# Performance work log

Hardware: AMD Instinct MI355X
Metric: run time of the kernel (lower is better)

## Reference

```python
import jax, jax.numpy as jnp
import numpy as np

N_NODES = 50000
N_EDGES = 800000
IN_DIM = 128
HID = 64
HEADS = 4
NEG_SLOPE = 0.2  # PyG GATConv default
EPS = 1e-16


def _glorot(key, shape):
    fan_in, fan_out = shape[0], shape[-1]
    lim = jnp.sqrt(6.0 / (fan_in + fan_out))
    return jax.random.uniform(key, shape, jnp.float32, -lim, lim)


def setup_inputs() -> dict:
    key = jax.random.key(0)
    ks = jax.random.split(key, 10)
    x = jax.random.normal(ks[0], (N_NODES, IN_DIM), jnp.float32)
    edge_index = jax.random.randint(ks[1], (2, N_EDGES), 0, N_NODES, jnp.int64)
    # Layer 1: in=128 -> 64 per head, 4 heads (concat -> 256)
    W1 = _glorot(ks[2], (IN_DIM, HEADS * HID))
    a_src1 = _glorot(ks[3], (HEADS, HID))
    a_dst1 = _glorot(ks[4], (HEADS, HID))
    b1 = jnp.zeros((HEADS * HID,), jnp.float32)
    # Layer 2: in=256 -> 1, 1 head
    W2 = _glorot(ks[5], (HEADS * HID, 1))
    a_src2 = _glorot(ks[6], (1, 1))
    a_dst2 = _glorot(ks[7], (1, 1))
    b2 = jnp.zeros((1,), jnp.float32)
    return {"x": x, "edge_index": edge_index, "W1": W1, "a_src1": a_src1,
            "a_dst1": a_dst1, "b1": b1, "W2": W2, "a_src2": a_src2,
            "a_dst2": a_dst2, "b2": b2}


def gat_conv(x, src, dst, W, a_src, a_dst, bias, heads, out_dim, num_nodes, concat):
    # Linear projection per head: [N, heads, out_dim]
    h = (x @ W).reshape(num_nodes, heads, out_dim)
    # Node-level attention logits: [N, heads]
    alpha_s = jnp.einsum('nhd,hd->nh', h, a_src)
    alpha_d = jnp.einsum('nhd,hd->nh', h, a_dst)
    # Per-edge score with LeakyReLU
    e = jax.nn.leaky_relu(alpha_s[src] + alpha_d[dst], NEG_SLOPE)  # [E, heads]
    # Segment softmax over incoming edges of each destination node
    e_max = jax.lax.stop_gradient(jax.ops.segment_max(e, dst, num_segments=num_nodes))
    e_exp = jnp.exp(e - e_max[dst])
    denom = jax.ops.segment_sum(e_exp, dst, num_segments=num_nodes)
    alpha = e_exp / (denom[dst] + EPS)  # [E, heads]
    # Weighted scatter-aggregate of source features
    msg = h[src] * alpha[:, :, None]  # [E, heads, out_dim]
    out = jax.ops.segment_sum(msg, dst, num_segments=num_nodes)
    if concat:
        out = out.reshape(num_nodes, heads * out_dim)
    else:
        out = out.mean(axis=1)
    return out + bias


def reference(x, edge_index, W1, a_src1, a_dst1, b1, W2, a_src2, a_dst2, b2):
    n = x.shape[0]
    loops = jnp.arange(n, dtype=edge_index.dtype)
    src = jnp.concatenate([edge_index[0], loops])  # PyG add_self_loops=True
    dst = jnp.concatenate([edge_index[1], loops])
    h = gat_conv(x, src, dst, W1, a_src1, a_dst1, b1, HEADS, HID, n, concat=True)
    h = jax.nn.relu(h)
    out = gat_conv(h, src, dst, W2, a_src2, a_dst2, b2, 1, 1, n, concat=True)
    return jax.nn.sigmoid(out)
```

## Files before the change

kernel.cpp:

```cpp
#include <hip/hip_runtime.h>
#include <hip/hip_bf16.h>

#define N_NODES 50000
#define N_EDGES 800000
#define ET      (N_EDGES + N_NODES)
#define IN_DIM  128
#define HID     64
#define HEADS   4
#define C1      (HEADS * HID)
#define NEG_SLOPE 0.2f

#define NBH     256
#define NBUCKET 196
#define SCAN_N  (NBUCKET * NBH)

typedef unsigned short ushort_t;
typedef __attribute__((ext_vector_type(8))) short bf16x8;
typedef __attribute__((ext_vector_type(4))) float f32x4;

__device__ __forceinline__ float asf(unsigned int u) {
    union { unsigned int i; float f; } c; c.i = u; return c.f;
}
__device__ __forceinline__ float bf2f(ushort_t u) {
    return asf(((unsigned int)u) << 16);
}
__device__ __forceinline__ ushort_t f2bf(float f) {
    union { float f; unsigned int i; } c; c.f = f;
    unsigned int r = c.i + 0x7fffu + ((c.i >> 16) & 1u);
    return (ushort_t)(r >> 16);
}
__device__ __forceinline__ float lrelu(float x) { return x > 0.f ? x : NEG_SLOPE * x; }

__device__ __forceinline__ float wave_sum(float v) {
    #pragma unroll
    for (int off = 32; off > 0; off >>= 1) v += __shfl_xor(v, off, 64);
    return v;
}
__device__ __forceinline__ int wave_sum_i(int v) {
    #pragma unroll
    for (int off = 32; off > 0; off >>= 1) v += __shfl_xor(v, off, 64);
    return v;
}

__device__ __forceinline__ int load_idx(const int* ei, int elem, int is64) {
    return is64 ? ei[2 * elem] : ei[elem];
}

__device__ __forceinline__ int detect64(const int* __restrict__ ei) {
    int lane = threadIdx.x & 63;
    unsigned long long nz = __ballot(lane < 32 && ei[2 * lane + 1] != 0);
    return nz == 0ull;
}

__global__ __launch_bounds__(256) void k_hist(const int* __restrict__ ei,
                                              int* __restrict__ HT) {
    __shared__ int lcnt[NBUCKET];
    int f = detect64(ei);
    if (threadIdx.x < NBUCKET) lcnt[threadIdx.x] = 0;
    __syncthreads();
    for (int e = blockIdx.x * 256 + threadIdx.x; e < ET; e += NBH * 256) {
        int d = (e < N_EDGES) ? load_idx(ei, N_EDGES + e, f) : e - N_EDGES;
        atomicAdd(&lcnt[d >> 8], 1);
    }
    __syncthreads();
    if (threadIdx.x < NBUCKET)
        HT[threadIdx.x * NBH + blockIdx.x] = lcnt[threadIdx.x];
}

__global__ __launch_bounds__(256) void k_blksum(const int* __restrict__ v,
                                                int* __restrict__ bsum) {
    int i = blockIdx.x * 256 + threadIdx.x;
    int s = wave_sum_i(v[i]);
    __shared__ int ws[4];
    int lane = threadIdx.x & 63, wid = threadIdx.x >> 6;
    if (lane == 0) ws[wid] = s;
    __syncthreads();
    if (threadIdx.x == 0) bsum[blockIdx.x] = ws[0] + ws[1] + ws[2] + ws[3];
}

__global__ __launch_bounds__(256) void k_bscan(const int* __restrict__ bsum,
                                               int* __restrict__ boff) {
    int tid = threadIdx.x, lane = tid & 63, wid = tid >> 6;
    int v = (tid < NBUCKET) ? bsum[tid] : 0;
    int x = v;
    #pragma unroll
    for (int off = 1; off < 64; off <<= 1) {
        int t = __shfl_up(x, off, 64);
        if (lane >= off) x += t;
    }
    __shared__ int ws[4];
    if (lane == 63) ws[wid] = x;
    __syncthreads();
    int add = 0;
    for (int w = 0; w < 4; ++w) if (w < wid) add += ws[w];
    x += add;
    if (tid < NBUCKET) boff[tid] = x - v;
}

__global__ __launch_bounds__(256) void k_apply(const int* __restrict__ v,
                                               const int* __restrict__ boff,
                                               int* __restrict__ out) {
    int i = blockIdx.x * 256 + threadIdx.x;
    int lane = threadIdx.x & 63, wid = threadIdx.x >> 6;
    int val = v[i];
    int x = val;
    #pragma unroll
    for (int off = 1; off < 64; off <<= 1) {
        int t = __shfl_up(x, off, 64);
        if (lane >= off) x += t;
    }
    __shared__ int ws[4];
    if (lane == 63) ws[wid] = x;
    __syncthreads();
    int add = boff[blockIdx.x];
    for (int w = 0; w < 4; ++w) if (w < wid) add += ws[w];
    out[i] = add + x - val;
}

__global__ __launch_bounds__(256) void k_bucket_scatter(const int* __restrict__ ei,
                                                        const int* __restrict__ HToff,
                                                        uint2* __restrict__ bucketed) {
    __shared__ int lbase[NBUCKET];
    int f = detect64(ei);
    if (threadIdx.x < NBUCKET)
        lbase[threadIdx.x] = HToff[threadIdx.x * NBH + blockIdx.x];
    __syncthreads();
    for (int e = blockIdx.x * 256 + threadIdx.x; e < ET; e += NBH * 256) {
        int s, d;
        if (e < N_EDGES) { s = load_idx(ei, e, f); d = load_idx(ei, N_EDGES + e, f); }
        else             { s = d = e - N_EDGES; }
        int pos = atomicAdd(&lbase[d >> 8], 1);
        bucketed[pos] = make_uint2((unsigned)s, (unsigned)d);
    }
}

__global__ __launch_bounds__(256) void k_fine(const uint2* __restrict__ bucketed,
                                              const int* __restrict__ HToff,
                                              int* __restrict__ row_start,
                                              int* __restrict__ edge_src) {
    __shared__ int fcnt[256];
    __shared__ int fcur[256];
    __shared__ int ws[4];
    int b = blockIdx.x, tid = threadIdx.x;
    int lane = tid & 63, wid = tid >> 6;
    int estart = HToff[b * NBH];
    int eend   = (b + 1 < NBUCKET) ? HToff[(b + 1) * NBH] : ET;
    fcnt[tid] = 0;
    __syncthreads();
    for (int i = estart + tid; i < eend; i += 256)
        atomicAdd(&fcnt[bucketed[i].y & 255], 1);
    __syncthreads();
    int v = fcnt[tid];
    int x = v;
    #pragma unroll
    for (int off = 1; off < 64; off <<= 1) {
        int t = __shfl_up(x, off, 64);
        if (lane >= off) x += t;
    }
    if (lane == 63) ws[wid] = x;
    __syncthreads();
    int add = 0;
    for (int w = 0; w < 4; ++w) if (w < wid) add += ws[w];
    int excl = add + x - v;
    int node = b * 256 + tid;
    if (node <= N_NODES) row_start[node] = estart + excl;
    fcur[tid] = estart + excl;
    __syncthreads();
    for (int i = estart + tid; i < eend; i += 256) {
        uint2 u = bucketed[i];
        int pos = atomicAdd(&fcur[u.y & 255], 1);
        edge_src[pos] = (int)u.x;
    }
}

__global__ void k_w1swz(const float* __restrict__ W1, ushort_t* __restrict__ w1s) {
    int o = blockIdx.x * 256 + threadIdx.x;
    int j = o & 7, l = (o >> 3) & 63, c = (o >> 9) & 3, t = o >> 11;
    int k = c * 32 + ((l >> 4) << 3) + j;
    int n = (t << 4) + (l & 15);
    w1s[o] = f2bf(W1[k * C1 + n]);
}

__global__ __launch_bounds__(256) void k_gemm1(const float* __restrict__ x,
                                               const ushort_t* __restrict__ w1s,
                                               const float* __restrict__ a_src1,
                                               const float* __restrict__ a_dst1,
                                               ushort_t* __restrict__ h1,
                                               float* __restrict__ as1,
                                               float* __restrict__ ad1) {
    int lane = threadIdx.x & 63;
    int wave = (blockIdx.x * 256 + threadIdx.x) >> 6;
    int row0 = wave * 16;
    if (row0 >= N_NODES) return;
    int quad = lane >> 4, mrow = lane & 15;

    f32x4 acc[16];
    #pragma unroll
    for (int t = 0; t < 16; ++t) acc[t] = (f32x4){0.f, 0.f, 0.f, 0.f};

    const float* xrow = x + (size_t)(row0 + mrow) * IN_DIM + quad * 8;
    #pragma unroll
    for (int c = 0; c < 4; ++c) {
        float4 xa = *(const float4*)(xrow + c * 32);
        float4 xb = *(const float4*)(xrow + c * 32 + 4);
        bf16x8 a;
        a[0] = (short)f2bf(xa.x); a[1] = (short)f2bf(xa.y);
        a[2] = (short)f2bf(xa.z); a[3] = (short)f2bf(xa.w);
        a[4] = (short)f2bf(xb.x); a[5] = (short)f2bf(xb.y);
        a[6] = (short)f2bf(xb.z); a[7] = (short)f2bf(xb.w);
        #pragma unroll
        for (int t = 0; t < 16; ++t) {
            bf16x8 b = *(const bf16x8*)(w1s + (((t * 4 + c) * 64 + lane) << 3));
            acc[t] = __builtin_amdgcn_mfma_f32_16x16x32_bf16(a, b, acc[t], 0, 0, 0);
        }
    }

    #pragma unroll
    for (int t = 0; t < 16; ++t) {
        int col = t * 16 + mrow;
        #pragma unroll
        for (int r = 0; r < 4; ++r) {
            h1[(size_t)(row0 + quad * 4 + r) * C1 + col] = f2bf(acc[t][r]);
        }
    }

    float asv[16], adv[16];
    #pragma unroll
    for (int t = 0; t < 16; ++t) {
        asv[t] = a_src1[t * 16 + mrow];
        adv[t] = a_dst1[t * 16 + mrow];
    }
    #pragma unroll
    for (int r = 0; r < 4; ++r) {
        float ps[4] = {0.f, 0.f, 0.f, 0.f};
        float pd[4] = {0.f, 0.f, 0.f, 0.f};
        #pragma unroll
        for (int t = 0; t < 16; ++t) {
            ps[t >> 2] += acc[t][r] * asv[t];
            pd[t >> 2] += acc[t][r] * adv[t];
        }
        #pragma unroll
        for (int h = 0; h < 4; ++h) {
            #pragma unroll
            for (int off = 1; off < 16; off <<= 1) {
                ps[h] += __shfl_xor(ps[h], off, 64);
                pd[h] += __shfl_xor(pd[h], off, 64);
            }
        }
        if (mrow == 0) {
            int rr = row0 + quad * 4 + r;
            #pragma unroll
            for (int h = 0; h < 4; ++h) {
                as1[rr * 4 + h] = ps[h];
                ad1[rr * 4 + h] = pd[h];
            }
        }
    }
}

__global__ __launch_bounds__(256) void k_agg1(const ushort_t* __restrict__ h1,
                                              const float* __restrict__ as1,
                                              const float* __restrict__ ad1,
                                              const int* __restrict__ row_start,
                                              const int* __restrict__ edge_src,
                                              const float* __restrict__ b1,
                                              const float* __restrict__ W2,
                                              const float* __restrict__ a_src2,
                                              const float* __restrict__ a_dst2,
                                              float2* __restrict__ pk,
                                              float* __restrict__ ad2) {
    __shared__ float wbuf[4][64][4];
    int lane = threadIdx.x & 63;
    int wid  = threadIdx.x >> 6;
    int node = blockIdx.x * 4 + wid;
    int rs = row_start[node], re = row_start[node + 1];
    float4 ad = *(const float4*)&ad1[node * 4];
    const int head = lane >> 4;

    float4 acc = make_float4(0.f, 0.f, 0.f, 0.f);
    float4 den = make_float4(0.f, 0.f, 0.f, 0.f);

    for (int base = rs; base < re; base += 64) {
        int i = base + lane;
        int s_l = 0;
        float4 w = make_float4(0.f, 0.f, 0.f, 0.f);
        if (i < re) {
            s_l = edge_src[i];
            float4 av = *(const float4*)&as1[s_l * 4];
            w.x = __expf(lrelu(av.x + ad.x));
            w.y = __expf(lrelu(av.y + ad.y));
            w.z = __expf(lrelu(av.z + ad.z));
            w.w = __expf(lrelu(av.w + ad.w));
        }
        den.x += w.x; den.y += w.y; den.z += w.z; den.w += w.w;
        *(float4*)&wbuf[wid][lane][0] = w;
        int m = re - base; if (m > 64) m = 64;
        int j = 0;
        for (; j + 4 <= m; j += 4) {
            int s0 = __builtin_amdgcn_readlane(s_l, j + 0);
            int s1 = __builtin_amdgcn_readlane(s_l, j + 1);
            int s2 = __builtin_amdgcn_readlane(s_l, j + 2);
            int s3 = __builtin_amdgcn_readlane(s_l, j + 3);
            uint2 p0 = *(const uint2*)(h1 + (size_t)s0 * C1 + lane * 4);
            uint2 p1 = *(const uint2*)(h1 + (size_t)s1 * C1 + lane * 4);
            uint2 p2 = *(const uint2*)(h1 + (size_t)s2 * C1 + lane * 4);
            uint2 p3 = *(const uint2*)(h1 + (size_t)s3 * C1 + lane * 4);
            float g0 = wbuf[wid][j + 0][head];
            float g1 = wbuf[wid][j + 1][head];
            float g2 = wbuf[wid][j + 2][head];
            float g3 = wbuf[wid][j + 3][head];
            acc.x += g0 * asf(p0.x << 16);
            acc.y += g0 * asf(p0.x & 0xffff0000u);
            acc.z += g0 * asf(p0.y << 16);
            acc.w += g0 * asf(p0.y & 0xffff0000u);
            acc.x += g1 * asf(p1.x << 16);
            acc.y += g1 * asf(p1.x & 0xffff0000u);
            acc.z += g1 * asf(p1.y << 16);
            acc.w += g1 * asf(p1.y & 0xffff0000u);
            acc.x += g2 * asf(p2.x << 16);
            acc.y += g2 * asf(p2.x & 0xffff0000u);
            acc.z += g2 * asf(p2.y << 16);
            acc.w += g2 * asf(p2.y & 0xffff0000u);
            acc.x += g3 * asf(p3.x << 16);
            acc.y += g3 * asf(p3.x & 0xffff0000u);
            acc.z += g3 * asf(p3.y << 16);
            acc.w += g3 * asf(p3.y & 0xffff0000u);
        }
        for (; j < m; ++j) {
            int s0 = __builtin_amdgcn_readlane(s_l, j);
            uint2 p0 = *(const uint2*)(h1 + (size_t)s0 * C1 + lane * 4);
            float g0 = wbuf[wid][j][head];
            acc.x += g0 * asf(p0.x << 16);
            acc.y += g0 * asf(p0.x & 0xffff0000u);
            acc.z += g0 * asf(p0.y << 16);
            acc.w += g0 * asf(p0.y & 0xffff0000u);
        }
    }

    float d0 = wave_sum(den.x), d1 = wave_sum(den.y);
    float d2 = wave_sum(den.z), d3 = wave_sum(den.w);
    float dh = head == 0 ? d0 : head == 1 ? d1 : head == 2 ? d2 : d3;
    float inv = 1.f / (dh + 1e-16f);
    float4 bv = *(const float4*)&b1[lane * 4];
    float o0 = fmaxf(acc.x * inv + bv.x, 0.f);
    float o1 = fmaxf(acc.y * inv + bv.y, 0.f);
    float o2 = fmaxf(acc.z * inv + bv.z, 0.f);
    float o3 = fmaxf(acc.w * inv + bv.w, 0.f);
    float4 wv = *(const float4*)&W2[lane * 4];
    float sum = o0 * wv.x + o1 * wv.y + o2 * wv.z + o3 * wv.w;
    sum = wave_sum(sum);
    if (lane == 0) {
        float2 p; p.x = sum * a_src2[0]; p.y = sum;
        pk[node]  = p;
        ad2[node] = sum * a_dst2[0];
    }
}

__global__ __launch_bounds__(256) void k_agg2(const float2* __restrict__ pk,
                                              const float* __restrict__ ad2,
                                              const int* __restrict__ row_start,
                                              const int* __restrict__ edge_src,
                                              const float* __restrict__ b2,
                                              float* __restrict__ outp) {
    int lane = threadIdx.x & 63;
    int node = blockIdx.x * 4 + (threadIdx.x >> 6);
    int rs = row_start[node], re = row_start[node + 1];
    float adv = ad2[node];
    float se = 0.f, wsm = 0.f;
    for (int i = rs + lane; i < re; i += 64) {
        int s = edge_src[i];
        float2 p = pk[s];
        float w = __expf(lrelu(p.x + adv));
        se += w; wsm += w * p.y;
    }
    se = wave_sum(se); wsm = wave_sum(wsm);
    if (lane == 0) {
        float v = wsm / (se + 1e-16f) + b2[0];
        outp[node] = 1.f / (1.f + __expf(-v));
    }
}

extern "C" void kernel_launch(void* const* d_in, const int* in_sizes, int n_in,
                              void* d_out, int out_size, void* d_ws, size_t ws_size,
                              hipStream_t stream) {
    (void)in_sizes; (void)n_in; (void)out_size; (void)ws_size;
    const float* x      = (const float*)d_in[0];
    const int*   ei     = (const int*)  d_in[1];
    const float* W1     = (const float*)d_in[2];
    const float* a_src1 = (const float*)d_in[3];
    const float* a_dst1 = (const float*)d_in[4];
    const float* b1     = (const float*)d_in[5];
    const float* W2     = (const float*)d_in[6];
    const float* a_src2 = (const float*)d_in[7];
    const float* a_dst2 = (const float*)d_in[8];
    const float* b2     = (const float*)d_in[9];
    float* out = (float*)d_out;

    char* w = (char*)d_ws;
    size_t off = 0;
    auto alloc = [&](size_t bytes) {
        void* p = w + off; off += (bytes + 255) & ~(size_t)255; return p;
    };
    ushort_t* h1       = (ushort_t*)alloc((size_t)N_NODES * C1 * 2);
    ushort_t* w1s      = (ushort_t*)alloc((size_t)IN_DIM * C1 * 2);
    float*    as1      = (float*)   alloc((size_t)N_NODES * 4 * 4);
    float*    ad1      = (float*)   alloc((size_t)N_NODES * 4 * 4);
    float2*   pk       = (float2*)  alloc((size_t)N_NODES * 8);
    float*    ad2      = (float*)   alloc((size_t)N_NODES * 4);
    int*      row_start= (int*)     alloc((size_t)(N_NODES + 1) * 4);
    int*      edge_src = (int*)     alloc((size_t)ET * 4);
    uint2*    bucketed = (uint2*)   alloc((size_t)ET * 8);
    int*      HT       = (int*)     alloc((size_t)SCAN_N * 4);
    int*      HToff    = (int*)     alloc((size_t)SCAN_N * 4);
    int*      bsum     = (int*)     alloc((size_t)NBUCKET * 4);
    int*      boff     = (int*)     alloc((size_t)NBUCKET * 4);

    k_hist<<<NBH, 256, 0, stream>>>(ei, HT);
    k_blksum<<<NBUCKET, 256, 0, stream>>>(HT, bsum);
    k_bscan<<<1, 256, 0, stream>>>(bsum, boff);
    k_apply<<<NBUCKET, 256, 0, stream>>>(HT, boff, HToff);
    k_bucket_scatter<<<NBH, 256, 0, stream>>>(ei, HToff, bucketed);
    k_fine<<<NBUCKET, 256, 0, stream>>>(bucketed, HToff, row_start, edge_src);

    k_w1swz<<<(IN_DIM * C1) / 256, 256, 0, stream>>>(W1, w1s);
    int nwave = (N_NODES + 15) / 16;
    k_gemm1<<<(nwave + 3) / 4, 256, 0, stream>>>(x, w1s, a_src1, a_dst1, h1, as1, ad1);
    k_agg1<<<N_NODES / 4, 256, 0, stream>>>(h1, as1, ad1, row_start, edge_src,
                                            b1, W2, a_src2, a_dst2, pk, ad2);
    k_agg2<<<N_NODES / 4, 256, 0, stream>>>(pk, ad2, row_start, edge_src, b2, out);
}
```

Before: 212.0 us.

## Precompute edge softmax weights in the CSR fine pass and fold the W1 swizzle into histogram

Edge attention weights (exp of leaky-relu logits) and per-node inverse softmax denominators are now computed inside k_fine, run after gemm1 with 512 threads. Each edge's four weights go to a float4 array; denominators are summed with LDS float atomics. k_agg1 then reads precomputed weights instead of gathering as1 and computing exp, and its inner gather loop is unrolled from 4 to 8. The W1 bf16 swizzle moves into k_hist to drop a launch. In exchange, roughly 27 MB of extra per-edge weight traffic is written and read back. k_fine, now running only 196 blocks, takes on the random as1 gathers and the atomics.

```diff
diff --git a/kernel.cpp b/kernel.cpp
--- a/kernel.cpp
+++ b/kernel.cpp
@@ -53,10 +53,19 @@
 }
 
 __global__ __launch_bounds__(256) void k_hist(const int* __restrict__ ei,
-                                              int* __restrict__ HT) {
+                                              int* __restrict__ HT,
+                                              const float* __restrict__ W1,
+                                              ushort_t* __restrict__ w1s) {
     __shared__ int lcnt[NBUCKET];
     int f = detect64(ei);
     if (threadIdx.x < NBUCKET) lcnt[threadIdx.x] = 0;
+    if (threadIdx.x < 128) {
+        int o = blockIdx.x * 128 + threadIdx.x;
+        int j = o & 7, l = (o >> 3) & 63, c = (o >> 9) & 3, t = o >> 11;
+        int k = c * 32 + ((l >> 4) << 3) + j;
+        int n = (t << 4) + (l & 15);
+        w1s[o] = f2bf(W1[k * C1 + n]);
+    }
     __syncthreads();
     for (int e = blockIdx.x * 256 + threadIdx.x; e < ET; e += NBH * 256) {
         int d = (e < N_EDGES) ? load_idx(ei, N_EDGES + e, f) : e - N_EDGES;
@@ -134,51 +143,81 @@
     }
 }
 
-__global__ __launch_bounds__(256) void k_fine(const uint2* __restrict__ bucketed,
+__global__ __launch_bounds__(512) void k_fine(const uint2* __restrict__ bucketed,
                                               const int* __restrict__ HToff,
+                                              const float* __restrict__ as1,
+                                              const float* __restrict__ ad1,
                                               int* __restrict__ row_start,
-                                              int* __restrict__ edge_src) {
+                                              int* __restrict__ edge_src,
+                                              float4* __restrict__ w4,
+                                              float* __restrict__ invden) {
     __shared__ int fcnt[256];
     __shared__ int fcur[256];
+    __shared__ float den[256][4];
     __shared__ int ws[4];
     int b = blockIdx.x, tid = threadIdx.x;
-    int lane = tid & 63, wid = tid >> 6;
     int estart = HToff[b * NBH];
     int eend   = (b + 1 < NBUCKET) ? HToff[(b + 1) * NBH] : ET;
-    fcnt[tid] = 0;
-    __syncthreads();
-    for (int i = estart + tid; i < eend; i += 256)
+    if (tid < 256) {
+        fcnt[tid] = 0;
+        den[tid][0] = 0.f; den[tid][1] = 0.f; den[tid][2] = 0.f; den[tid][3] = 0.f;
+    }
+    __syncthreads();
+    for (int i = estart + tid; i < eend; i += 512)
         atomicAdd(&fcnt[bucketed[i].y & 255], 1);
     __syncthreads();
-    int v = fcnt[tid];
-    int x = v;
-    #pragma unroll
-    for (int off = 1; off < 64; off <<= 1) {
-        int t = __shfl_up(x, off, 64);
-        if (lane >= off) x += t;
-    }
-    if (lane == 63) ws[wid] = x;
-    __syncthreads();
-    int add = 0;
-    for (int w = 0; w < 4; ++w) if (w < wid) add += ws[w];
-    int excl = add + x - v;
-    int node = b * 256 + tid;
-    if (node <= N_NODES) row_start[node] = estart + excl;
-    fcur[tid] = estart + excl;
-    __syncthreads();
-    for (int i = estart + tid; i < eend; i += 256) {
+    if (tid < 256) {
+        int lane = tid & 63, wid = tid >> 6;
+        int v = fcnt[tid];
+        int x = v;
+        #pragma unroll
+        for (int off = 1; off < 64; off <<= 1) {
+            int t = __shfl_up(x, off, 64);
+            if (lane >= off) x += t;
+        }
+        if (lane == 63) ws[wid] = x;
+        __syncthreads();
+        int add = 0;
+        for (int w = 0; w < 4; ++w) if (w < wid) add += ws[w];
+        int excl = add + x - v;
+        int node = b * 256 + tid;
+        if (node <= N_NODES) row_start[node] = estart + excl;
+        fcur[tid] = estart + excl;
+    } else {
+        __syncthreads();
+    }
+    __syncthreads();
+    for (int i = estart + tid; i < eend; i += 512) {
         uint2 u = bucketed[i];
-        int pos = atomicAdd(&fcur[u.y & 255], 1);
-        edge_src[pos] = (int)u.x;
-    }
-}
-
-__global__ void k_w1swz(const float* __restrict__ W1, ushort_t* __restrict__ w1s) {
-    int o = blockIdx.x * 256 + threadIdx.x;
-    int j = o & 7, l = (o >> 3) & 63, c = (o >> 9) & 3, t = o >> 11;
-    int k = c * 32 + ((l >> 4) << 3) + j;
-    int n = (t << 4) + (l & 15);
-    w1s[o] = f2bf(W1[k * C1 + n]);
+        int loc = u.y & 255;
+        int pos = atomicAdd(&fcur[loc], 1);
+        int s = (int)u.x;
+        float4 av = *(const float4*)&as1[s * 4];
+        float4 dv = *(const float4*)&ad1[(size_t)u.y * 4];
+        float4 wv;
+        wv.x = __expf(lrelu(av.x + dv.x));
+        wv.y = __expf(lrelu(av.y + dv.y));
+        wv.z = __expf(lrelu(av.z + dv.z));
+        wv.w = __expf(lrelu(av.w + dv.w));
+        w4[pos] = wv;
+        edge_src[pos] = s;
+        atomicAdd(&den[loc][0], wv.x);
+        atomicAdd(&den[loc][1], wv.y);
+        atomicAdd(&den[loc][2], wv.z);
+        atomicAdd(&den[loc][3], wv.w);
+    }
+    __syncthreads();
+    if (tid < 256) {
+        int node = b * 256 + tid;
+        if (node < N_NODES) {
+            float4 iv;
+            iv.x = 1.f / (den[tid][0] + 1e-16f);
+            iv.y = 1.f / (den[tid][1] + 1e-16f);
+            iv.z = 1.f / (den[tid][2] + 1e-16f);
+            iv.w = 1.f / (den[tid][3] + 1e-16f);
+            *(float4*)&invden[(size_t)node * 4] = iv;
+        }
+    }
 }
 
 __global__ __launch_bounds__(256) void k_gemm1(const float* __restrict__ x,
@@ -259,10 +298,10 @@
 }
 
 __global__ __launch_bounds__(256) void k_agg1(const ushort_t* __restrict__ h1,
-                                              const float* __restrict__ as1,
-                                              const float* __restrict__ ad1,
                                               const int* __restrict__ row_start,
                                               const int* __restrict__ edge_src,
+                                              const float4* __restrict__ w4,
+                                              const float* __restrict__ invden,
                                               const float* __restrict__ b1,
                                               const float* __restrict__ W2,
                                               const float* __restrict__ a_src2,
@@ -274,57 +313,34 @@
     int wid  = threadIdx.x >> 6;
     int node = blockIdx.x * 4 + wid;
     int rs = row_start[node], re = row_start[node + 1];
-    float4 ad = *(const float4*)&ad1[node * 4];
     const int head = lane >> 4;
 
     float4 acc = make_float4(0.f, 0.f, 0.f, 0.f);
-    float4 den = make_float4(0.f, 0.f, 0.f, 0.f);
 
     for (int base = rs; base < re; base += 64) {
         int i = base + lane;
         int s_l = 0;
-        float4 w = make_float4(0.f, 0.f, 0.f, 0.f);
-        if (i < re) {
-            s_l = edge_src[i];
-            float4 av = *(const float4*)&as1[s_l * 4];
-            w.x = __expf(lrelu(av.x + ad.x));
-            w.y = __expf(lrelu(av.y + ad.y));
-            w.z = __expf(lrelu(av.z + ad.z));
-            w.w = __expf(lrelu(av.w + ad.w));
-        }
-        den.x += w.x; den.y += w.y; den.z += w.z; den.w += w.w;
-        *(float4*)&wbuf[wid][lane][0] = w;
+        float4 wv = make_float4(0.f, 0.f, 0.f, 0.f);
+        if (i < re) { s_l = edge_src[i]; wv = w4[i]; }
+        *(float4*)&wbuf[wid][lane][0] = wv;
         int m = re - base; if (m > 64) m = 64;
         int j = 0;
-        for (; j + 4 <= m; j += 4) {
-            int s0 = __builtin_amdgcn_readlane(s_l, j + 0);
-            int s1 = __builtin_amdgcn_readlane(s_l, j + 1);
-            int s2 = __builtin_amdgcn_readlane(s_l, j + 2);
-            int s3 = __builtin_amdgcn_readlane(s_l, j + 3);
-            uint2 p0 = *(const uint2*)(h1 + (size_t)s0 * C1 + lane * 4);
-            uint2 p1 = *(const uint2*)(h1 + (size_t)s1 * C1 + lane * 4);
-            uint2 p2 = *(const uint2*)(h1 + (size_t)s2 * C1 + lane * 4);
-            uint2 p3 = *(const uint2*)(h1 + (size_t)s3 * C1 + lane * 4);
-            float g0 = wbuf[wid][j + 0][head];
-            float g1 = wbuf[wid][j + 1][head];
-            float g2 = wbuf[wid][j + 2][head];
-            float g3 = wbuf[wid][j + 3][head];
-            acc.x += g0 * asf(p0.x << 16);
-            acc.y += g0 * asf(p0.x & 0xffff0000u);
-            acc.z += g0 * asf(p0.y << 16);
-            acc.w += g0 * asf(p0.y & 0xffff0000u);
-            acc.x += g1 * asf(p1.x << 16);
-            acc.y += g1 * asf(p1.x & 0xffff0000u);
-            acc.z += g1 * asf(p1.y << 16);
-            acc.w += g1 * asf(p1.y & 0xffff0000u);
-            acc.x += g2 * asf(p2.x << 16);
-            acc.y += g2 * asf(p2.x & 0xffff0000u);
-            acc.z += g2 * asf(p2.y << 16);
-            acc.w += g2 * asf(p2.y & 0xffff0000u);
-            acc.x += g3 * asf(p3.x << 16);
-            acc.y += g3 * asf(p3.x & 0xffff0000u);
-            acc.z += g3 * asf(p3.y << 16);
-            acc.w += g3 * asf(p3.y & 0xffff0000u);
+        for (; j + 8 <= m; j += 8) {
+            int ss[8]; uint2 pp[8]; float gg[8];
+            #pragma unroll
+            for (int q = 0; q < 8; ++q) ss[q] = __builtin_amdgcn_readlane(s_l, j + q);
+            #pragma unroll
+            for (int q = 0; q < 8; ++q) {
+                pp[q] = *(const uint2*)(h1 + (size_t)ss[q] * C1 + lane * 4);
+                gg[q] = wbuf[wid][j + q][head];
+            }
+            #pragma unroll
+            for (int q = 0; q < 8; ++q) {
+                acc.x += gg[q] * asf(pp[q].x << 16);
+                acc.y += gg[q] * asf(pp[q].x & 0xffff0000u);
+                acc.z += gg[q] * asf(pp[q].y << 16);
+                acc.w += gg[q] * asf(pp[q].y & 0xffff0000u);
+            }
         }
         for (; j < m; ++j) {
             int s0 = __builtin_amdgcn_readlane(s_l, j);
@@ -337,17 +353,14 @@
         }
     }
 
-    float d0 = wave_sum(den.x), d1 = wave_sum(den.y);
-    float d2 = wave_sum(den.z), d3 = wave_sum(den.w);
-    float dh = head == 0 ? d0 : head == 1 ? d1 : head == 2 ? d2 : d3;
-    float inv = 1.f / (dh + 1e-16f);
+    float inv = invden[(size_t)node * 4 + head];
     float4 bv = *(const float4*)&b1[lane * 4];
     float o0 = fmaxf(acc.x * inv + bv.x, 0.f);
     float o1 = fmaxf(acc.y * inv + bv.y, 0.f);
     float o2 = fmaxf(acc.z * inv + bv.z, 0.f);
     float o3 = fmaxf(acc.w * inv + bv.w, 0.f);
-    float4 wv = *(const float4*)&W2[lane * 4];
-    float sum = o0 * wv.x + o1 * wv.y + o2 * wv.z + o3 * wv.w;
+    float4 wv2 = *(const float4*)&W2[lane * 4];
+    float sum = o0 * wv2.x + o1 * wv2.y + o2 * wv2.z + o3 * wv2.w;
     sum = wave_sum(sum);
     if (lane == 0) {
         float2 p; p.x = sum * a_src2[0]; p.y = sum;
@@ -405,27 +418,29 @@
     ushort_t* w1s      = (ushort_t*)alloc((size_t)IN_DIM * C1 * 2);
     float*    as1      = (float*)   alloc((size_t)N_NODES * 4 * 4);
     float*    ad1      = (float*)   alloc((size_t)N_NODES * 4 * 4);
+    float*    invden   = (float*)   alloc((size_t)N_NODES * 4 * 4);
     float2*   pk       = (float2*)  alloc((size_t)N_NODES * 8);
     float*    ad2      = (float*)   alloc((size_t)N_NODES * 4);
     int*      row_start= (int*)     alloc((size_t)(N_NODES + 1) * 4);
     int*      edge_src = (int*)     alloc((size_t)ET * 4);
+    float4*   w4       = (float4*)  alloc((size_t)ET * 16);
     uint2*    bucketed = (uint2*)   alloc((size_t)ET * 8);
     int*      HT       = (int*)     alloc((size_t)SCAN_N * 4);
     int*      HToff    = (int*)     alloc((size_t)SCAN_N * 4);
     int*      bsum     = (int*)     alloc((size_t)NBUCKET * 4);
     int*      boff     = (int*)     alloc((size_t)NBUCKET * 4);
 
-    k_hist<<<NBH, 256, 0, stream>>>(ei, HT);
+    k_hist<<<NBH, 256, 0, stream>>>(ei, HT, W1, w1s);
     k_blksum<<<NBUCKET, 256, 0, stream>>>(HT, bsum);
     k_bscan<<<1, 256, 0, stream>>>(bsum, boff);
     k_apply<<<NBUCKET, 256, 0, stream>>>(HT, boff, HToff);
     k_bucket_scatter<<<NBH, 256, 0, stream>>>(ei, HToff, bucketed);
-    k_fine<<<NBUCKET, 256, 0, stream>>>(bucketed, HToff, row_start, edge_src);
-
-    k_w1swz<<<(IN_DIM * C1) / 256, 256, 0, stream>>>(W1, w1s);
+
     int nwave = (N_NODES + 15) / 16;
     k_gemm1<<<(nwave + 3) / 4, 256, 0, stream>>>(x, w1s, a_src1, a_dst1, h1, as1, ad1);
-    k_agg1<<<N_NODES / 4, 256, 0, stream>>>(h1, as1, ad1, row_start, edge_src,
+    k_fine<<<NBUCKET, 512, 0, stream>>>(bucketed, HToff, as1, ad1,
+                                        row_start, edge_src, w4, invden);
+    k_agg1<<<N_NODES / 4, 256, 0, stream>>>(h1, row_start, edge_src, w4, invden,
                                             b1, W2, a_src2, a_dst2, pk, ad2);
     k_agg2<<<N_NODES / 4, 256, 0, stream>>>(pk, ad2, row_start, edge_src, b2, out);
 }
```

New measurement: 224.2 us. +5.8%, slower.

## Split agg1 gather into half-waves with 16-byte loads; fold W1 swizzle into histogram

Applied to the files above, without the earlier changes.

The layer-1 aggregation now assigns each half-wave to a different edge. Each lane loads 8 bf16 features with a 16-byte load, so a wave gathers two source rows per step and keeps up to eight edges in flight per unrolled iteration. The two halves' partial sums are combined with a cross-half shuffle, and the final wave sum is halved to undo the duplication. Separately, the W1 bf16 swizzle is moved into the histogram kernel to remove one launch. The odd-edge tail reads padding lanes that carry zero weight, which costs extra loads but keeps the result correct.

```diff
diff --git a/kernel.cpp b/kernel.cpp
--- a/kernel.cpp
+++ b/kernel.cpp
@@ -53,10 +53,19 @@
 }
 
 __global__ __launch_bounds__(256) void k_hist(const int* __restrict__ ei,
-                                              int* __restrict__ HT) {
+                                              int* __restrict__ HT,
+                                              const float* __restrict__ W1,
+                                              ushort_t* __restrict__ w1s) {
     __shared__ int lcnt[NBUCKET];
     int f = detect64(ei);
     if (threadIdx.x < NBUCKET) lcnt[threadIdx.x] = 0;
+    if (threadIdx.x < 128) {
+        int o = blockIdx.x * 128 + threadIdx.x;
+        int j = o & 7, l = (o >> 3) & 63, c = (o >> 9) & 3, t = o >> 11;
+        int k = c * 32 + ((l >> 4) << 3) + j;
+        int n = (t << 4) + (l & 15);
+        w1s[o] = f2bf(W1[k * C1 + n]);
+    }
     __syncthreads();
     for (int e = blockIdx.x * 256 + threadIdx.x; e < ET; e += NBH * 256) {
         int d = (e < N_EDGES) ? load_idx(ei, N_EDGES + e, f) : e - N_EDGES;
@@ -171,14 +180,6 @@
         int pos = atomicAdd(&fcur[u.y & 255], 1);
         edge_src[pos] = (int)u.x;
     }
-}
-
-__global__ void k_w1swz(const float* __restrict__ W1, ushort_t* __restrict__ w1s) {
-    int o = blockIdx.x * 256 + threadIdx.x;
-    int j = o & 7, l = (o >> 3) & 63, c = (o >> 9) & 3, t = o >> 11;
-    int k = c * 32 + ((l >> 4) << 3) + j;
-    int n = (t << 4) + (l & 15);
-    w1s[o] = f2bf(W1[k * C1 + n]);
 }
 
 __global__ __launch_bounds__(256) void k_gemm1(const float* __restrict__ x,
@@ -275,9 +276,11 @@
     int node = blockIdx.x * 4 + wid;
     int rs = row_start[node], re = row_start[node + 1];
     float4 ad = *(const float4*)&ad1[node * 4];
-    const int head = lane >> 4;
-
-    float4 acc = make_float4(0.f, 0.f, 0.f, 0.f);
+    const int lane32 = lane & 31;
+    const int half   = lane >> 5;
+    const int head8  = lane32 >> 3;
+
+    float acc[8] = {0.f, 0.f, 0.f, 0.f, 0.f, 0.f, 0.f, 0.f};
     float4 den = make_float4(0.f, 0.f, 0.f, 0.f);
 
     for (int base = rs; base < re; base += 64) {
@@ -296,59 +299,71 @@
         *(float4*)&wbuf[wid][lane][0] = w;
         int m = re - base; if (m > 64) m = 64;
         int j = 0;
-        for (; j + 4 <= m; j += 4) {
-            int s0 = __builtin_amdgcn_readlane(s_l, j + 0);
+        for (; j + 8 <= m; j += 8) {
+            int sp[4]; uint4 pp[4]; float gg[4];
+            #pragma unroll
+            for (int q = 0; q < 4; ++q) {
+                int s0 = __builtin_amdgcn_readlane(s_l, j + 2 * q);
+                int s1 = __builtin_amdgcn_readlane(s_l, j + 2 * q + 1);
+                sp[q] = half ? s1 : s0;
+            }
+            #pragma unroll
+            for (int q = 0; q < 4; ++q) {
+                pp[q] = *(const uint4*)(h1 + (size_t)sp[q] * C1 + lane32 * 8);
+                gg[q] = wbuf[wid][j + 2 * q + half][head8];
+            }
+            #pragma unroll
+            for (int q = 0; q < 4; ++q) {
+                acc[0] += gg[q] * asf(pp[q].x << 16);
+                acc[1] += gg[q] * asf(pp[q].x & 0xffff0000u);
+                acc[2] += gg[q] * asf(pp[q].y << 16);
+                acc[3] += gg[q] * asf(pp[q].y & 0xffff0000u);
+                acc[4] += gg[q] * asf(pp[q].z << 16);
+                acc[5] += gg[q] * asf(pp[q].z & 0xffff0000u);
+                acc[6] += gg[q] * asf(pp[q].w << 16);
+                acc[7] += gg[q] * asf(pp[q].w & 0xffff0000u);
+            }
+        }
+        for (; j < m; j += 2) {
+            int s0 = __builtin_amdgcn_readlane(s_l, j);
             int s1 = __builtin_amdgcn_readlane(s_l, j + 1);
-            int s2 = __builtin_amdgcn_readlane(s_l, j + 2);
-            int s3 = __builtin_amdgcn_readlane(s_l, j + 3);
-            uint2 p0 = *(const uint2*)(h1 + (size_t)s0 * C1 + lane * 4);
-            uint2 p1 = *(const uint2*)(h1 + (size_t)s1 * C1 + lane * 4);
-            uint2 p2 = *(const uint2*)(h1 + (size_t)s2 * C1 + lane * 4);
-            uint2 p3 = *(const uint2*)(h1 + (size_t)s3 * C1 + lane * 4);
-            float g0 = wbuf[wid][j + 0][head];
-            float g1 = wbuf[wid][j + 1][head];
-            float g2 = wbuf[wid][j + 2][head];
-            float g3 = wbuf[wid][j + 3][head];
-            acc.x += g0 * asf(p0.x << 16);
-            acc.y += g0 * asf(p0.x & 0xffff0000u);
-            acc.z += g0 * asf(p0.y << 16);
-            acc.w += g0 * asf(p0.y & 0xffff0000u);
-            acc.x += g1 * asf(p1.x << 16);
-            acc.y += g1 * asf(p1.x & 0xffff0000u);
-            acc.z += g1 * asf(p1.y << 16);
-            acc.w += g1 * asf(p1.y & 0xffff0000u);
-            acc.x += g2 * asf(p2.x << 16);
-            acc.y += g2 * asf(p2.x & 0xffff0000u);
-            acc.z += g2 * asf(p2.y << 16);
-            acc.w += g2 * asf(p2.y & 0xffff0000u);
-            acc.x += g3 * asf(p3.x << 16);
-            acc.y += g3 * asf(p3.x & 0xffff0000u);
-            acc.z += g3 * asf(p3.y << 16);
-            acc.w += g3 * asf(p3.y & 0xffff0000u);
-        }
-        for (; j < m; ++j) {
-            int s0 = __builtin_amdgcn_readlane(s_l, j);
-            uint2 p0 = *(const uint2*)(h1 + (size_t)s0 * C1 + lane * 4);
-            float g0 = wbuf[wid][j][head];
-            acc.x += g0 * asf(p0.x << 16);
-            acc.y += g0 * asf(p0.x & 0xffff0000u);
-            acc.z += g0 * asf(p0.y << 16);
-            acc.w += g0 * asf(p0.y & 0xffff0000u);
-        }
-    }
+            int sp = half ? s1 : s0;
+            uint4 p0 = *(const uint4*)(h1 + (size_t)sp * C1 + lane32 * 8);
+            float g0 = wbuf[wid][j + half][head8];
+            acc[0] += g0 * asf(p0.x << 16);
+            acc[1] += g0 * asf(p0.x & 0xffff0000u);
+            acc[2] += g0 * asf(p0.y << 16);
+            acc[3] += g0 * asf(p0.y & 0xffff0000u);
+            acc[4] += g0 * asf(p0.z << 16);
+            acc[5] += g0 * asf(p0.z & 0xffff0000u);
+            acc[6] += g0 * asf(p0.w << 16);
+            acc[7] += g0 * asf(p0.w & 0xffff0000u);
+        }
+    }
+
+    #pragma unroll
+    for (int i2 = 0; i2 < 8; ++i2) acc[i2] += __shfl_xor(acc[i2], 32, 64);
 
     float d0 = wave_sum(den.x), d1 = wave_sum(den.y);
     float d2 = wave_sum(den.z), d3 = wave_sum(den.w);
-    float dh = head == 0 ? d0 : head == 1 ? d1 : head == 2 ? d2 : d3;
+    float dh = head8 == 0 ? d0 : head8 == 1 ? d1 : head8 == 2 ? d2 : d3;
     float inv = 1.f / (dh + 1e-16f);
-    float4 bv = *(const float4*)&b1[lane * 4];
-    float o0 = fmaxf(acc.x * inv + bv.x, 0.f);
-    float o1 = fmaxf(acc.y * inv + bv.y, 0.f);
-    float o2 = fmaxf(acc.z * inv + bv.z, 0.f);
-    float o3 = fmaxf(acc.w * inv + bv.w, 0.f);
-    float4 wv = *(const float4*)&W2[lane * 4];
-    float sum = o0 * wv.x + o1 * wv.y + o2 * wv.z + o3 * wv.w;
-    sum = wave_sum(sum);
+    float4 bva = *(const float4*)&b1[lane32 * 8];
+    float4 bvb = *(const float4*)&b1[lane32 * 8 + 4];
+    float o[8];
+    o[0] = fmaxf(acc[0] * inv + bva.x, 0.f);
+    o[1] = fmaxf(acc[1] * inv + bva.y, 0.f);
+    o[2] = fmaxf(acc[2] * inv + bva.z, 0.f);
+    o[3] = fmaxf(acc[3] * inv + bva.w, 0.f);
+    o[4] = fmaxf(acc[4] * inv + bvb.x, 0.f);
+    o[5] = fmaxf(acc[5] * inv + bvb.y, 0.f);
+    o[6] = fmaxf(acc[6] * inv + bvb.z, 0.f);
+    o[7] = fmaxf(acc[7] * inv + bvb.w, 0.f);
+    float4 wva = *(const float4*)&W2[lane32 * 8];
+    float4 wvb = *(const float4*)&W2[lane32 * 8 + 4];
+    float sum = o[0] * wva.x + o[1] * wva.y + o[2] * wva.z + o[3] * wva.w
+              + o[4] * wvb.x + o[5] * wvb.y + o[6] * wvb.z + o[7] * wvb.w;
+    sum = wave_sum(sum) * 0.5f;
     if (lane == 0) {
         float2 p; p.x = sum * a_src2[0]; p.y = sum;
         pk[node]  = p;
@@ -415,14 +430,13 @@
     int*      bsum     = (int*)     alloc((size_t)NBUCKET * 4);
     int*      boff     = (int*)     alloc((size_t)NBUCKET * 4);
 
-    k_hist<<<NBH, 256, 0, stream>>>(ei, HT);
+    k_hist<<<NBH, 256, 0, stream>>>(ei, HT, W1, w1s);
     k_blksum<<<NBUCKET, 256, 0, stream>>>(HT, bsum);
     k_bscan<<<1, 256, 0, stream>>>(bsum, boff);
     k_apply<<<NBUCKET, 256, 0, stream>>>(HT, boff, HToff);
     k_bucket_scatter<<<NBH, 256, 0, stream>>>(ei, HToff, bucketed);
     k_fine<<<NBUCKET, 256, 0, stream>>>(bucketed, HToff, row_start, edge_src);
 
-    k_w1swz<<<(IN_DIM * C1) / 256, 256, 0, stream>>>(W1, w1s);
     int nwave = (N_NODES + 15) / 16;
     k_gemm1<<<(nwave + 3) / 4, 256, 0, stream>>>(x, w1s, a_src1, a_dst1, h1, as1, ad1);
     k_agg1<<<N_NODES / 4, 256, 0, stream>>>(h1, as1, ad1, row_start, edge_src,
```

Measured after the change: 213.6 us. No clear change (+0.8%).
